# Performance work log

Measured on AMD Instinct MI355X. Metric: run time of the kernel, lower is better.

## Reference

```python
import jax, jax.numpy as jnp
import numpy as np

H = 256      # hidden_size (hardcoded by view([-1,1,256]) in the torch source)
V = 50257    # output_size / vocab
L = 50       # max_length


def gru_cell(x, h, w_ih, w_hh, b_ih, b_hh):
    """PyTorch GRUCell semantics. x, h: [H]; w_*: [3H, H]; b_*: [3H]."""
    gi = w_ih @ x + b_ih
    gh = w_hh @ h + b_hh
    gi_r, gi_z, gi_n = jnp.split(gi, 3)
    gh_r, gh_z, gh_n = jnp.split(gh, 3)
    r = jax.nn.sigmoid(gi_r + gh_r)
    z = jax.nn.sigmoid(gi_z + gh_z)
    n = jnp.tanh(gi_n + r * gh_n)
    return (1.0 - z) * n + z * h


def setup_inputs() -> dict:
    key = jax.random.key(0)
    ks = jax.random.split(key, 24)
    p = lambda k, shape: (0.02 * jax.random.normal(k, shape)).astype(jnp.float32)
    d = {}
    d["token"] = jax.random.randint(ks[0], (1,), 0, V)
    d["hidden"] = jax.random.normal(ks[1], (1, 1, H), dtype=jnp.float32)
    d["encoder_outputs"] = jax.random.normal(ks[2], (L, H), dtype=jnp.float32)
    d["emb"] = p(ks[3], (V, H))
    d["attn_W"] = p(ks[4], (L, 2 * H)); d["attn_b"] = jnp.zeros((L,), jnp.float32)
    d["comb_W"] = p(ks[5], (H, 2 * H)); d["comb_b"] = jnp.zeros((H,), jnp.float32)
    # bidirectional GRU: forward (f) and reverse (b) direction weights
    d["w_ih_f"] = p(ks[6], (3 * H, H)); d["w_hh_f"] = p(ks[7], (3 * H, H))
    d["b_ih_f"] = jnp.zeros((3 * H,), jnp.float32); d["b_hh_f"] = jnp.zeros((3 * H,), jnp.float32)
    d["w_ih_b"] = p(ks[8], (3 * H, H)); d["w_hh_b"] = p(ks[9], (3 * H, H))
    d["b_ih_b"] = jnp.zeros((3 * H,), jnp.float32); d["b_hh_b"] = jnp.zeros((3 * H,), jnp.float32)
    # second (unidirectional) GRU
    d["w_ih_g"] = p(ks[10], (3 * H, H)); d["w_hh_g"] = p(ks[11], (3 * H, H))
    d["b_ih_g"] = jnp.zeros((3 * H,), jnp.float32); d["b_hh_g"] = jnp.zeros((3 * H,), jnp.float32)
    d["out_W"] = p(ks[12], (V, H)); d["out_b"] = jnp.zeros((V,), jnp.float32)
    return d


def reference(token, hidden, encoder_outputs, emb, attn_W, attn_b, comb_W, comb_b,
              w_ih_f, w_hh_f, b_ih_f, b_hh_f, w_ih_b, w_hh_b, b_ih_b, b_hh_b,
              w_ih_g, w_hh_g, b_ih_g, b_hh_g, out_W, out_b):
    # dropout is treated as identity (eval mode)
    e = emb[token[0]]                       # [H] embedded token
    h0 = hidden[0, 0]                       # [H]
    # attention weights over encoder positions
    aw = jax.nn.softmax(jax.nn.relu(attn_W @ jnp.concatenate([e, h0]) + attn_b))  # [L]
    applied = aw @ encoder_outputs          # [H]
    x = jax.nn.relu(comb_W @ jnp.concatenate([e, applied]) + comb_b)              # [H]
    # bidirectional GRU, seq_len=1: both directions see the same step, init hidden = h0
    hf = gru_cell(x, h0, w_ih_f, w_hh_f, b_ih_f, b_hh_f)
    hb = gru_cell(x, h0, w_ih_b, w_hh_b, b_ih_b, b_hh_b)
    hm = 0.5 * (hf + hb)                    # torch.mean(bihidden, dim=0)
    # bioutput (1,1,512) viewed as (2,1,256) -> second GRU runs 2 steps
    h1 = gru_cell(hf, hm, w_ih_g, w_hh_g, b_ih_g, b_hh_g)
    h2 = gru_cell(hb, h1, w_ih_g, w_hh_g, b_ih_g, b_hh_g)
    logp = jax.nn.log_softmax(out_W @ h1 + out_b)  # output[0] = first timestep = h1
    return (logp[None, :], h2[None, None, :], aw[None, :])
```

## Files before the change

### kernel.cpp

```cpp
#include <hip/hip_runtime.h>
#include <math.h>

#define H 256
#define L 50
#define V 50257
#define LOGIT_BLKS 786

__device__ __forceinline__ float dot4(float4 a, float4 b) {
    return a.x * b.x + a.y * b.y + a.z * b.z + a.w * b.w;
}

__device__ __forceinline__ float wave_reduce_sum(float v) {
#pragma unroll
    for (int m = 32; m >= 1; m >>= 1) v += __shfl_xor(v, m, 64);
    return v;
}

__device__ __forceinline__ float wave_reduce_max(float v) {
#pragma unroll
    for (int m = 32; m >= 1; m >>= 1) v = fmaxf(v, __shfl_xor(v, m, 64));
    return v;
}

__device__ __forceinline__ float sigmoidf(float x) { return 1.0f / (1.0f + __expf(-x)); }

__device__ __forceinline__ void ms_push(float& m, float& s, float x) {
    float mn = fmaxf(m, x);
    s = s * __expf(m - mn) + __expf(x - mn);
    m = mn;
}
__device__ __forceinline__ void ms_merge(float& m, float& s, float om, float os) {
    float M = fmaxf(m, om);
    float a = (m == -INFINITY) ? 0.f : s * __expf(m - M);
    float c = (om == -INFINITY) ? 0.f : os * __expf(om - M);
    m = M; s = a + c;
}

__device__ __forceinline__ void gru_wave(
    int j, int lane, float4 xv, float4 hv, float hj,
    const float* __restrict__ w_ih, const float* __restrict__ w_hh,
    const float* __restrict__ b_ih, const float* __restrict__ b_hh,
    float* __restrict__ outp)
{
    float gi[3], gh[3];
#pragma unroll
    for (int k = 0; k < 3; ++k) {
        int row = k * H + j;
        const float4* wi4 = (const float4*)(w_ih + (size_t)row * H);
        const float4* wh4 = (const float4*)(w_hh + (size_t)row * H);
        gi[k] = wave_reduce_sum(dot4(wi4[lane], xv)) + b_ih[row];
        gh[k] = wave_reduce_sum(dot4(wh4[lane], hv)) + b_hh[row];
    }
    if (lane == 0) {
        float r = sigmoidf(gi[0] + gh[0]);
        float z = sigmoidf(gi[1] + gh[1]);
        float n = tanhf(gi[2] + r * gh[2]);
        outp[j] = (1.f - z) * n + z * hj;
    }
}

__global__ __launch_bounds__(256) void k_scores(
    const int* __restrict__ token, const float* __restrict__ hidden,
    const float* __restrict__ emb, const float* __restrict__ attn_W,
    const float* __restrict__ attn_b, float* __restrict__ ws_scores)
{
    __shared__ float s_vec[2 * H];
    int t = threadIdx.x, wid = t >> 6, lane = t & 63;
    int tok = token[0];
    s_vec[t] = emb[(size_t)tok * H + t];
    s_vec[H + t] = hidden[t];
    __syncthreads();
    int row = blockIdx.x * 4 + wid;
    if (row < L) {
        float acc = 0.f;
#pragma unroll
        for (int c = 0; c < 8; ++c)
            acc += attn_W[row * 2 * H + c * 64 + lane] * s_vec[c * 64 + lane];
        acc = wave_reduce_sum(acc);
        if (lane == 0) ws_scores[row] = fmaxf(acc + attn_b[row], 0.f);
    }
}

__global__ __launch_bounds__(256) void k_comb(
    const int* __restrict__ token, const float* __restrict__ emb,
    const float* __restrict__ enc, const float* __restrict__ comb_W,
    const float* __restrict__ comb_b, const float* __restrict__ ws_scores,
    float* __restrict__ ws_x, float* __restrict__ out_aw)
{
    __shared__ __align__(16) float s_cat[2 * H];
    __shared__ float s_aw[64];
    int t = threadIdx.x, wid = t >> 6, lane = t & 63;
    int tok = token[0];
    s_cat[t] = emb[(size_t)tok * H + t];
    if (t < 64) {
        float v = (t < L) ? ws_scores[t] : -INFINITY;
        float mx = wave_reduce_max(v);
        float e = (t < L) ? __expf(v - mx) : 0.f;
        float ssum = wave_reduce_sum(e);
        if (t < L) {
            float aw = e / ssum;
            s_aw[t] = aw;
            if (blockIdx.x == 0) out_aw[t] = aw;
        }
    }
    __syncthreads();
    float app = 0.f;
    for (int l = 0; l < L; ++l) app += s_aw[l] * enc[l * H + t];
    s_cat[H + t] = app;
    __syncthreads();
    int row = blockIdx.x * 4 + wid;
    const float4* c4 = (const float4*)s_cat;
    const float4* W4 = (const float4*)(comb_W + (size_t)row * 2 * H);
    float acc = dot4(W4[lane], c4[lane]) + dot4(W4[lane + 64], c4[lane + 64]);
    acc = wave_reduce_sum(acc);
    if (lane == 0) ws_x[row] = fmaxf(acc + comb_b[row], 0.f);
}

__global__ __launch_bounds__(256) void k_gru_fb(
    const float* __restrict__ ws_x, const float* __restrict__ hidden,
    const float* __restrict__ w_ih_f, const float* __restrict__ w_hh_f,
    const float* __restrict__ b_ih_f, const float* __restrict__ b_hh_f,
    const float* __restrict__ w_ih_b, const float* __restrict__ w_hh_b,
    const float* __restrict__ b_ih_b, const float* __restrict__ b_hh_b,
    float* __restrict__ ws_hf, float* __restrict__ ws_hb)
{
    int t = threadIdx.x, wid = t >> 6, lane = t & 63;
    int g = blockIdx.x * 4 + wid;
    int dir = g >> 8, j = g & 255;
    gru_wave(j, lane, ((const float4*)ws_x)[lane], ((const float4*)hidden)[lane],
             hidden[j],
             dir ? w_ih_b : w_ih_f, dir ? w_hh_b : w_hh_f,
             dir ? b_ih_b : b_ih_f, dir ? b_hh_b : b_hh_f,
             dir ? ws_hb : ws_hf);
}

__global__ __launch_bounds__(256) void k_gru(
    const float* __restrict__ xvec, const float* __restrict__ ha,
    const float* __restrict__ hb,
    const float* __restrict__ w_ih, const float* __restrict__ w_hh,
    const float* __restrict__ b_ih, const float* __restrict__ b_hh,
    float* __restrict__ outp)
{
    int t = threadIdx.x, wid = t >> 6, lane = t & 63;
    int j = blockIdx.x * 4 + wid;
    float4 xv = ((const float4*)xvec)[lane];
    float4 hv = ((const float4*)ha)[lane];
    float hj;
    if (hb) {
        float4 bv = ((const float4*)hb)[lane];
        hv = make_float4(0.5f * (hv.x + bv.x), 0.5f * (hv.y + bv.y),
                         0.5f * (hv.z + bv.z), 0.5f * (hv.w + bv.w));
        hj = 0.5f * (ha[j] + hb[j]);
    } else {
        hj = ha[j];
    }
    gru_wave(j, lane, xv, hv, hj, w_ih, w_hh, b_ih, b_hh, outp);
}

__global__ __launch_bounds__(256) void k_logits(
    const float* __restrict__ out_W, const float* __restrict__ out_b,
    const float* __restrict__ h1, float* __restrict__ logits,
    float* __restrict__ part_m, float* __restrict__ part_s)
{
    __shared__ float s_m4[4], s_s4[4];
    int t = threadIdx.x, wid = t >> 6, lane = t & 63;
    float4 hv = ((const float4*)h1)[lane];
    int base = (blockIdx.x * 4 + wid) * 16;
    float m = -INFINITY, s = 0.f;
#pragma unroll 1
    for (int k = 0; k < 16; k += 2) {
        int v = base + k;
        if (v >= V) break;
        const float4* W0 = (const float4*)(out_W + (size_t)v * H);
        float4 a0 = W0[lane];
        bool has2 = (v + 1 < V);
        float4 a1 = has2 ? ((const float4*)(out_W + (size_t)(v + 1) * H))[lane]
                         : make_float4(0.f, 0.f, 0.f, 0.f);
        float x0 = wave_reduce_sum(dot4(a0, hv)) + out_b[v];
        float x1 = wave_reduce_sum(dot4(a1, hv));
        if (lane == 0) logits[v] = x0;
        ms_push(m, s, x0);
        if (has2) {
            x1 += out_b[v + 1];
            if (lane == 0) logits[v + 1] = x1;
            ms_push(m, s, x1);
        }
    }
    if (lane == 0) { s_m4[wid] = m; s_s4[wid] = s; }
    __syncthreads();
    if (t == 0) {
        float M = s_m4[0], S = s_s4[0];
#pragma unroll
        for (int q = 1; q < 4; ++q) ms_merge(M, S, s_m4[q], s_s4[q]);
        part_m[blockIdx.x] = M; part_s[blockIdx.x] = S;
    }
}

__global__ __launch_bounds__(256) void k_final(
    const float* __restrict__ part_m, const float* __restrict__ part_s,
    float* __restrict__ logits)
{
    __shared__ float s_m4[4], s_s4[4];
    __shared__ float s_bcast;
    int t = threadIdx.x, wid = t >> 6, lane = t & 63;
    float m = -INFINITY, s = 0.f;
    for (int idx = t; idx < LOGIT_BLKS; idx += 256)
        ms_merge(m, s, part_m[idx], part_s[idx]);
#pragma unroll
    for (int d = 32; d >= 1; d >>= 1) {
        float om = __shfl_xor(m, d, 64);
        float os = __shfl_xor(s, d, 64);
        ms_merge(m, s, om, os);
    }
    if (lane == 0) { s_m4[wid] = m; s_s4[wid] = s; }
    __syncthreads();
    if (t == 0) {
        float M = s_m4[0], S = s_s4[0];
#pragma unroll
        for (int q = 1; q < 4; ++q) ms_merge(M, S, s_m4[q], s_s4[q]);
        s_bcast = M + logf(S);
    }
    __syncthreads();
    float lse = s_bcast;
    int i = blockIdx.x * 256 + t;
    if (i < V) logits[i] -= lse;
}

extern "C" void kernel_launch(void* const* d_in, const int* in_sizes, int n_in,
                              void* d_out, int out_size, void* d_ws, size_t ws_size,
                              hipStream_t stream)
{
    const int*   token  = (const int*)d_in[0];
    const float* hidden = (const float*)d_in[1];
    const float* enc    = (const float*)d_in[2];
    const float* emb    = (const float*)d_in[3];
    const float* attn_W = (const float*)d_in[4];
    const float* attn_b = (const float*)d_in[5];
    const float* comb_W = (const float*)d_in[6];
    const float* comb_b = (const float*)d_in[7];
    const float* w_ih_f = (const float*)d_in[8];
    const float* w_hh_f = (const float*)d_in[9];
    const float* b_ih_f = (const float*)d_in[10];
    const float* b_hh_f = (const float*)d_in[11];
    const float* w_ih_b = (const float*)d_in[12];
    const float* w_hh_b = (const float*)d_in[13];
    const float* b_ih_b = (const float*)d_in[14];
    const float* b_hh_b = (const float*)d_in[15];
    const float* w_ih_g = (const float*)d_in[16];
    const float* w_hh_g = (const float*)d_in[17];
    const float* b_ih_g = (const float*)d_in[18];
    const float* b_hh_g = (const float*)d_in[19];
    const float* out_W  = (const float*)d_in[20];
    const float* out_b  = (const float*)d_in[21];

    float* out = (float*)d_out;
    float* ws  = (float*)d_ws;
    float* ws_scores = ws;
    float* ws_x      = ws + 64;
    float* ws_hf     = ws + 320;
    float* ws_hb     = ws + 576;
    float* ws_h1     = ws + 832;
    float* part_m    = ws + 1088;
    float* part_s    = ws + 1888;

    k_scores<<<13, 256, 0, stream>>>(token, hidden, emb, attn_W, attn_b, ws_scores);
    k_comb<<<64, 256, 0, stream>>>(token, emb, enc, comb_W, comb_b, ws_scores,
                                   ws_x, out + V + H);
    k_gru_fb<<<128, 256, 0, stream>>>(ws_x, hidden,
                                      w_ih_f, w_hh_f, b_ih_f, b_hh_f,
                                      w_ih_b, w_hh_b, b_ih_b, b_hh_b,
                                      ws_hf, ws_hb);
    k_gru<<<64, 256, 0, stream>>>(ws_hf, ws_hf, ws_hb,
                                  w_ih_g, w_hh_g, b_ih_g, b_hh_g, ws_h1);
    k_gru<<<64, 256, 0, stream>>>(ws_hb, ws_h1, nullptr,
                                  w_ih_g, w_hh_g, b_ih_g, b_hh_g, out + V);
    k_logits<<<LOGIT_BLKS, 256, 0, stream>>>(out_W, out_b, ws_h1, out,
                                             part_m, part_s);
    k_final<<<197, 256, 0, stream>>>(part_m, part_s, out);
}
```

Before: 177.8 us.

## Prefetch output weights into cache during GRU stages and fuse small kernels

Merges the attention-score kernel into the combine kernel, folds the second GRU step into the logits launch as extra blocks, and adds idle blocks to the early dependent kernels. Those blocks stream slices of the large output weight matrix, about 2.5M float4, into cache so the later logits pass finds it warm. The aim is to overlap the bandwidth-bound weight read with the latency-bound serial GRU chain and to cut launch count. The cost is extra redundant traffic and a dependence on the last-level cache being large enough to hold the prefetched data. It also adds sink writes to workspace.

```diff
diff --git a/kernel.cpp b/kernel.cpp
--- a/kernel.cpp
+++ b/kernel.cpp
@@ -5,6 +5,8 @@
 #define L 50
 #define V 50257
 #define LOGIT_BLKS 786
+#define H2_BLKS 64
+#define TOTAL4 (V * H / 4)
 
 __device__ __forceinline__ float dot4(float4 a, float4 b) {
     return a.x * b.x + a.y * b.y + a.z * b.z + a.w * b.w;
@@ -34,6 +36,20 @@
     float a = (m == -INFINITY) ? 0.f : s * __expf(m - M);
     float c = (om == -INFINITY) ? 0.f : os * __expf(om - M);
     m = M; s = a + c;
+}
+
+__device__ __forceinline__ void prefetch_slice(
+    const float4* __restrict__ w4, int beg4, int fin4, float* __restrict__ sink,
+    int slot)
+{
+    int t = threadIdx.x, lane = t & 63;
+    float acc = 0.f;
+    for (int i = beg4 + t; i < fin4; i += 256) {
+        float4 q = w4[i];
+        acc += q.x + q.y + q.z + q.w;
+    }
+    acc = wave_reduce_sum(acc);
+    if (lane == 0) sink[slot] = acc;
 }
 
 __device__ __forceinline__ void gru_wave(
@@ -59,73 +75,82 @@
     }
 }
 
-__global__ __launch_bounds__(256) void k_scores(
+#define PF1 1000000
+__global__ __launch_bounds__(256) void k_comb(
     const int* __restrict__ token, const float* __restrict__ hidden,
-    const float* __restrict__ emb, const float* __restrict__ attn_W,
-    const float* __restrict__ attn_b, float* __restrict__ ws_scores)
-{
-    __shared__ float s_vec[2 * H];
-    int t = threadIdx.x, wid = t >> 6, lane = t & 63;
+    const float* __restrict__ emb, const float* __restrict__ enc,
+    const float* __restrict__ attn_W, const float* __restrict__ attn_b,
+    const float* __restrict__ comb_W, const float* __restrict__ comb_b,
+    const float* __restrict__ out_W,
+    float* __restrict__ ws_x, float* __restrict__ out_aw, float* __restrict__ sink)
+{
+    int b = blockIdx.x, t = threadIdx.x, wid = t >> 6, lane = t & 63;
+    if (b >= 64) {
+        int i = b - 64;
+        const int per = (PF1 + 447) / 448;
+        prefetch_slice((const float4*)out_W, i * per, min(PF1, (i + 1) * per),
+                       sink, b * 4 + wid);
+        return;
+    }
+    __shared__ __align__(16) float s_eh[2 * H];
+    __shared__ float s_scores[L];
+    __shared__ float s_aw[64];
     int tok = token[0];
-    s_vec[t] = emb[(size_t)tok * H + t];
-    s_vec[H + t] = hidden[t];
-    __syncthreads();
-    int row = blockIdx.x * 4 + wid;
-    if (row < L) {
+    s_eh[t] = emb[(size_t)tok * H + t];
+    s_eh[H + t] = hidden[t];
+    __syncthreads();
+    for (int l = wid; l < L; l += 4) {
         float acc = 0.f;
 #pragma unroll
         for (int c = 0; c < 8; ++c)
-            acc += attn_W[row * 2 * H + c * 64 + lane] * s_vec[c * 64 + lane];
+            acc += attn_W[l * 2 * H + c * 64 + lane] * s_eh[c * 64 + lane];
         acc = wave_reduce_sum(acc);
-        if (lane == 0) ws_scores[row] = fmaxf(acc + attn_b[row], 0.f);
-    }
-}
-
-__global__ __launch_bounds__(256) void k_comb(
-    const int* __restrict__ token, const float* __restrict__ emb,
-    const float* __restrict__ enc, const float* __restrict__ comb_W,
-    const float* __restrict__ comb_b, const float* __restrict__ ws_scores,
-    float* __restrict__ ws_x, float* __restrict__ out_aw)
-{
-    __shared__ __align__(16) float s_cat[2 * H];
-    __shared__ float s_aw[64];
-    int t = threadIdx.x, wid = t >> 6, lane = t & 63;
-    int tok = token[0];
-    s_cat[t] = emb[(size_t)tok * H + t];
+        if (lane == 0) s_scores[l] = fmaxf(acc + attn_b[l], 0.f);
+    }
+    __syncthreads();
     if (t < 64) {
-        float v = (t < L) ? ws_scores[t] : -INFINITY;
+        float v = (t < L) ? s_scores[t] : -INFINITY;
         float mx = wave_reduce_max(v);
         float e = (t < L) ? __expf(v - mx) : 0.f;
         float ssum = wave_reduce_sum(e);
         if (t < L) {
             float aw = e / ssum;
             s_aw[t] = aw;
-            if (blockIdx.x == 0) out_aw[t] = aw;
+            if (b == 0) out_aw[t] = aw;
         }
     }
     __syncthreads();
     float app = 0.f;
     for (int l = 0; l < L; ++l) app += s_aw[l] * enc[l * H + t];
-    s_cat[H + t] = app;
-    __syncthreads();
-    int row = blockIdx.x * 4 + wid;
-    const float4* c4 = (const float4*)s_cat;
+    s_eh[H + t] = app;
+    __syncthreads();
+    int row = b * 4 + wid;
+    const float4* c4 = (const float4*)s_eh;
     const float4* W4 = (const float4*)(comb_W + (size_t)row * 2 * H);
     float acc = dot4(W4[lane], c4[lane]) + dot4(W4[lane + 64], c4[lane + 64]);
     acc = wave_reduce_sum(acc);
     if (lane == 0) ws_x[row] = fmaxf(acc + comb_b[row], 0.f);
 }
 
+#define PF2 1000000
 __global__ __launch_bounds__(256) void k_gru_fb(
     const float* __restrict__ ws_x, const float* __restrict__ hidden,
     const float* __restrict__ w_ih_f, const float* __restrict__ w_hh_f,
     const float* __restrict__ b_ih_f, const float* __restrict__ b_hh_f,
     const float* __restrict__ w_ih_b, const float* __restrict__ w_hh_b,
     const float* __restrict__ b_ih_b, const float* __restrict__ b_hh_b,
-    float* __restrict__ ws_hf, float* __restrict__ ws_hb)
-{
-    int t = threadIdx.x, wid = t >> 6, lane = t & 63;
-    int g = blockIdx.x * 4 + wid;
+    const float* __restrict__ out_W,
+    float* __restrict__ ws_hf, float* __restrict__ ws_hb, float* __restrict__ sink)
+{
+    int b = blockIdx.x, t = threadIdx.x, wid = t >> 6, lane = t & 63;
+    if (b >= 128) {
+        int i = b - 128;
+        const int per = (PF2 + 383) / 384;
+        prefetch_slice((const float4*)out_W, PF1 + i * per,
+                       PF1 + min(PF2, (i + 1) * per), sink, b * 4 + wid);
+        return;
+    }
+    int g = b * 4 + wid;
     int dir = g >> 8, j = g & 255;
     gru_wave(j, lane, ((const float4*)ws_x)[lane], ((const float4*)hidden)[lane],
              hidden[j],
@@ -134,38 +159,49 @@
              dir ? ws_hb : ws_hf);
 }
 
-__global__ __launch_bounds__(256) void k_gru(
-    const float* __restrict__ xvec, const float* __restrict__ ha,
-    const float* __restrict__ hb,
-    const float* __restrict__ w_ih, const float* __restrict__ w_hh,
-    const float* __restrict__ b_ih, const float* __restrict__ b_hh,
-    float* __restrict__ outp)
-{
-    int t = threadIdx.x, wid = t >> 6, lane = t & 63;
-    int j = blockIdx.x * 4 + wid;
-    float4 xv = ((const float4*)xvec)[lane];
-    float4 hv = ((const float4*)ha)[lane];
-    float hj;
-    if (hb) {
-        float4 bv = ((const float4*)hb)[lane];
-        hv = make_float4(0.5f * (hv.x + bv.x), 0.5f * (hv.y + bv.y),
-                         0.5f * (hv.z + bv.z), 0.5f * (hv.w + bv.w));
-        hj = 0.5f * (ha[j] + hb[j]);
-    } else {
-        hj = ha[j];
-    }
-    gru_wave(j, lane, xv, hv, hj, w_ih, w_hh, b_ih, b_hh, outp);
+#define PF3 500000
+__global__ __launch_bounds__(256) void k_gru1(
+    const float* __restrict__ ws_hf, const float* __restrict__ ws_hb,
+    const float* __restrict__ w_ih_g, const float* __restrict__ w_hh_g,
+    const float* __restrict__ b_ih_g, const float* __restrict__ b_hh_g,
+    const float* __restrict__ out_W,
+    float* __restrict__ ws_h1, float* __restrict__ sink)
+{
+    int b = blockIdx.x, t = threadIdx.x, wid = t >> 6, lane = t & 63;
+    if (b >= 64) {
+        int i = b - 64;
+        const int per = (PF3 + 447) / 448;
+        prefetch_slice((const float4*)out_W, PF1 + PF2 + i * per,
+                       PF1 + PF2 + min(PF3, (i + 1) * per), sink, b * 4 + wid);
+        return;
+    }
+    int j = b * 4 + wid;
+    float4 av = ((const float4*)ws_hf)[lane];
+    float4 bv = ((const float4*)ws_hb)[lane];
+    float4 hv = make_float4(0.5f * (av.x + bv.x), 0.5f * (av.y + bv.y),
+                            0.5f * (av.z + bv.z), 0.5f * (av.w + bv.w));
+    float hj = 0.5f * (ws_hf[j] + ws_hb[j]);
+    gru_wave(j, lane, av, hv, hj, w_ih_g, w_hh_g, b_ih_g, b_hh_g, ws_h1);
 }
 
 __global__ __launch_bounds__(256) void k_logits(
     const float* __restrict__ out_W, const float* __restrict__ out_b,
-    const float* __restrict__ h1, float* __restrict__ logits,
+    const float* __restrict__ h1, const float* __restrict__ ws_hb,
+    const float* __restrict__ w_ih_g, const float* __restrict__ w_hh_g,
+    const float* __restrict__ b_ih_g, const float* __restrict__ b_hh_g,
+    float* __restrict__ logits, float* __restrict__ out_h2,
     float* __restrict__ part_m, float* __restrict__ part_s)
 {
+    int b = blockIdx.x, t = threadIdx.x, wid = t >> 6, lane = t & 63;
+    if (b >= LOGIT_BLKS) {
+        int j = (b - LOGIT_BLKS) * 4 + wid;
+        gru_wave(j, lane, ((const float4*)ws_hb)[lane], ((const float4*)h1)[lane],
+                 h1[j], w_ih_g, w_hh_g, b_ih_g, b_hh_g, out_h2);
+        return;
+    }
     __shared__ float s_m4[4], s_s4[4];
-    int t = threadIdx.x, wid = t >> 6, lane = t & 63;
     float4 hv = ((const float4*)h1)[lane];
-    int base = (blockIdx.x * 4 + wid) * 16;
+    int base = (b * 4 + wid) * 16;
     float m = -INFINITY, s = 0.f;
 #pragma unroll 1
     for (int k = 0; k < 16; k += 2) {
@@ -192,7 +228,7 @@
         float M = s_m4[0], S = s_s4[0];
 #pragma unroll
         for (int q = 1; q < 4; ++q) ms_merge(M, S, s_m4[q], s_s4[q]);
-        part_m[blockIdx.x] = M; part_s[blockIdx.x] = S;
+        part_m[b] = M; part_s[b] = S;
     }
 }
 
@@ -255,26 +291,25 @@
 
     float* out = (float*)d_out;
     float* ws  = (float*)d_ws;
-    float* ws_scores = ws;
-    float* ws_x      = ws + 64;
-    float* ws_hf     = ws + 320;
-    float* ws_hb     = ws + 576;
-    float* ws_h1     = ws + 832;
-    float* part_m    = ws + 1088;
-    float* part_s    = ws + 1888;
-
-    k_scores<<<13, 256, 0, stream>>>(token, hidden, emb, attn_W, attn_b, ws_scores);
-    k_comb<<<64, 256, 0, stream>>>(token, emb, enc, comb_W, comb_b, ws_scores,
-                                   ws_x, out + V + H);
-    k_gru_fb<<<128, 256, 0, stream>>>(ws_x, hidden,
+    float* ws_x   = ws;
+    float* ws_hf  = ws + 256;
+    float* ws_hb  = ws + 512;
+    float* ws_h1  = ws + 768;
+    float* part_m = ws + 1088;
+    float* part_s = ws + 1888;
+    float* sink   = ws + 4096;
+
+    k_comb<<<512, 256, 0, stream>>>(token, hidden, emb, enc, attn_W, attn_b,
+                                    comb_W, comb_b, out_W, ws_x, out + V + H, sink);
+    k_gru_fb<<<512, 256, 0, stream>>>(ws_x, hidden,
                                       w_ih_f, w_hh_f, b_ih_f, b_hh_f,
                                       w_ih_b, w_hh_b, b_ih_b, b_hh_b,
-                                      ws_hf, ws_hb);
-    k_gru<<<64, 256, 0, stream>>>(ws_hf, ws_hf, ws_hb,
-                                  w_ih_g, w_hh_g, b_ih_g, b_hh_g, ws_h1);
-    k_gru<<<64, 256, 0, stream>>>(ws_hb, ws_h1, nullptr,
-                                  w_ih_g, w_hh_g, b_ih_g, b_hh_g, out + V);
-    k_logits<<<LOGIT_BLKS, 256, 0, stream>>>(out_W, out_b, ws_h1, out,
-                                             part_m, part_s);
+                                      out_W, ws_hf, ws_hb, sink);
+    k_gru1<<<512, 256, 0, stream>>>(ws_hf, ws_hb,
+                                    w_ih_g, w_hh_g, b_ih_g, b_hh_g,
+                                    out_W, ws_h1, sink);
+    k_logits<<<LOGIT_BLKS + H2_BLKS, 256, 0, stream>>>(
+        out_W, out_b, ws_h1, ws_hb, w_ih_g, w_hh_g, b_ih_g, b_hh_g,
+        out, out + V, part_m, part_s);
     k_final<<<197, 256, 0, stream>>>(part_m, part_s, out);
 }
```

Measured after the change: 189.9 us. 6.8% more time.
